# Kernel optimization log

Hardware: AMD Instinct MI355X
Metric: run time of the kernel (lower is better)

## Reference

```python
import jax, jax.numpy as jnp
import numpy as np

NEG_FILL = jnp.finfo(jnp.float32).min  # stands in for tf.float64.min (overflows to -inf in f32)


def setup_inputs() -> dict:
    key = jax.random.key(0)
    k0, k1, k2, k3, k4 = jax.random.split(key, 5)
    B, N, E, D = 4, 4096, 1024, 256
    STD = 0.05  # tf.random_normal_initializer default stddev
    inputs = jax.random.normal(k0, (B, N, E), dtype=jnp.float32)
    Wq = STD * jax.random.normal(k1, (E, D), dtype=jnp.float32)
    Wk = STD * jax.random.normal(k2, (E, D), dtype=jnp.float32)
    Wvdown = STD * jax.random.normal(k3, (E, D), dtype=jnp.float32)
    Wvup = STD * jax.random.normal(k4, (D, E), dtype=jnp.float32)
    return {"inputs": inputs, "Wq": Wq, "Wk": Wk, "Wvdown": Wvdown, "Wvup": Wvup}


def reference(inputs, Wq, Wk, Wvdown, Wvup):
    B, N, E = inputs.shape
    D = Wq.shape[1]
    Q = inputs @ Wq                                   # [B, N, D]
    K = inputs @ Wk                                   # [B, N, D]
    score = jnp.einsum("bqd,bkd->bqk", Q, K)          # [B, N, N]
    score = score / jnp.sqrt(jnp.float32(D))
    # tf.linalg.band_part(score, -1, 0): keep lower triangle (causal)
    causal = jnp.tril(jnp.ones((N, N), dtype=bool))
    score = jnp.where(causal, score, 0.0)
    # original quirk: any exactly-zero entry (including masked ones) -> huge negative
    score = jnp.where(score != 0, score, NEG_FILL)
    attn = jax.nn.softmax(score, axis=-1)             # [B, N, N]
    V = inputs @ (Wvdown @ Wvup)                      # low-rank value proj, [B, N, E]
    return attn @ V                                   # [B, N, E]
```

## Files before the change

### kernel.cpp

```cpp
#include <hip/hip_runtime.h>
#include <hip/hip_bf16.h>


typedef __hip_bfloat16 bf16;
typedef __bf16 bf16x4 __attribute__((ext_vector_type(4)));
typedef __bf16 bf16x8 __attribute__((ext_vector_type(8)));
typedef float f32x4 __attribute__((ext_vector_type(4)));

#define BK 32

__device__ __forceinline__ void gload_lds16(const bf16* g, bf16* l) {
    __builtin_amdgcn_global_load_lds(
        (const __attribute__((address_space(1))) unsigned int*)g,
        (__attribute__((address_space(3))) unsigned int*)l, 16, 0, 0);
}

__device__ __forceinline__ void zero_acc(f32x4 acc[4][4]) {
#pragma unroll
    for (int mi = 0; mi < 4; ++mi)
#pragma unroll
        for (int ni = 0; ni < 4; ++ni) {
            f32x4 zf = {0.f, 0.f, 0.f, 0.f};
            acc[mi][ni] = zf;
        }
}

__device__ __forceinline__ void mm_tile(const bf16* __restrict__ Ablk,
                                        const bf16* __restrict__ Bblk,
                                        int lda, int ldb, int kiters,
                                        bf16* As, bf16* Bs, f32x4 acc[4][4]) {
    const int tid  = threadIdx.x;
    const int wave = tid >> 6;
    const int lane = tid & 63;

    const int F0 = wave * 2048 + lane * 16;
    const int F1 = F0 + 1024;
    const int r0 = F0 >> 6, c0 = (F0 & 63) >> 1;
    const int r1 = F1 >> 6, c1 = (F1 & 63) >> 1;
    const bf16* ga0 = Ablk + (size_t)r0 * lda + c0;
    const bf16* ga1 = Ablk + (size_t)r1 * lda + c1;
    const bf16* gb0 = Bblk + (size_t)r0 * ldb + c0;
    const bf16* gb1 = Bblk + (size_t)r1 * ldb + c1;
    bf16* lA0 = (bf16*)((char*)As + F0);
    bf16* lA1 = (bf16*)((char*)As + F1);
    bf16* lB0 = (bf16*)((char*)Bs + F0);
    bf16* lB1 = (bf16*)((char*)Bs + F1);

    const int waveM = wave >> 1, waveN = wave & 1;
    const int mrow = waveM * 64 + (lane & 15);
    const int nrow = waveN * 64 + (lane & 15);
    const int koff = (lane >> 4) * 8;

    for (int it = 0; it < kiters; ++it) {
        gload_lds16(ga0, lA0);
        gload_lds16(ga1, lA1);
        gload_lds16(gb0, lB0);
        gload_lds16(gb1, lB1);
        ga0 += BK; ga1 += BK; gb0 += BK; gb1 += BK;
        __syncthreads();

        bf16x8 af[4], bfr[4];
#pragma unroll
        for (int mi = 0; mi < 4; ++mi)
            af[mi] = *(const bf16x8*)(As + (mrow + mi * 16) * BK + koff);
#pragma unroll
        for (int ni = 0; ni < 4; ++ni)
            bfr[ni] = *(const bf16x8*)(Bs + (nrow + ni * 16) * BK + koff);
#pragma unroll
        for (int mi = 0; mi < 4; ++mi)
#pragma unroll
            for (int ni = 0; ni < 4; ++ni)
                acc[mi][ni] = __builtin_amdgcn_mfma_f32_16x16x32_bf16(
                    af[mi], bfr[ni], acc[mi][ni], 0, 0, 0);
        __syncthreads();
    }
}

__global__ __launch_bounds__(256, 2) void k_gemm_plain(
    const bf16* __restrict__ A, long long aBatch,
    const bf16* __restrict__ BT, long long bBatch,
    bf16* __restrict__ C, long long cBatch,
    int lda, int ldb, int ldc, int kiters) {
    __shared__ __align__(16) bf16 As[128 * BK];
    __shared__ __align__(16) bf16 Bs[128 * BK];
    const int nBase = blockIdx.x * 128;
    const int mBase = blockIdx.y * 128;
    const int z = blockIdx.z;
    const bf16* Ab = A + (size_t)z * aBatch + (size_t)mBase * lda;
    const bf16* Bb = BT + (size_t)z * bBatch + (size_t)nBase * ldb;

    f32x4 acc[4][4];
    zero_acc(acc);
    mm_tile(Ab, Bb, lda, ldb, kiters, As, Bs, acc);

    const int tid = threadIdx.x, wave = tid >> 6, lane = tid & 63;
    const int waveM = wave >> 1, waveN = wave & 1;
    const int quad = lane >> 4, cno = lane & 15;
    bf16* Cb = C + (size_t)z * cBatch;
#pragma unroll
    for (int mi = 0; mi < 4; ++mi) {
        int row0 = mBase + waveM * 64 + mi * 16 + quad * 4;
#pragma unroll
        for (int ni = 0; ni < 4; ++ni) {
            int col = nBase + waveN * 64 + ni * 16 + cno;
#pragma unroll
            for (int r = 0; r < 4; ++r)
                Cb[(size_t)(row0 + r) * ldc + col] = __float2bfloat16(acc[mi][ni][r]);
        }
    }
}

#define P_BATCH 8650752ll
__global__ __launch_bounds__(256, 2) void k_score(
    const bf16* __restrict__ Qm, const bf16* __restrict__ Km,
    bf16* __restrict__ P, float* __restrict__ lsum) {
    const int f = blockIdx.x, b = blockIdx.z;
    int qt = (int)((sqrtf(8.f * (float)f + 1.f) - 1.f) * 0.5f);
    while ((qt + 1) * (qt + 2) / 2 <= f) ++qt;
    while (qt * (qt + 1) / 2 > f) --qt;
    const int kt = f - qt * (qt + 1) / 2;

    __shared__ __align__(16) bf16 As[128 * BK];
    __shared__ __align__(16) bf16 Bs[128 * BK];

    const bf16* Ab = Qm + ((size_t)b * 4096 + (size_t)qt * 128) * 256;
    const bf16* Bb = Km + ((size_t)b * 4096 + (size_t)kt * 128) * 256;

    f32x4 acc[4][4];
    zero_acc(acc);
    mm_tile(Ab, Bb, 256, 256, 256 / BK, As, Bs, acc);

    const int tid = threadIdx.x, wave = tid >> 6, lane = tid & 63;
    const int waveM = wave >> 1, waveN = wave & 1;
    const int quad = lane >> 4, cno = lane & 15;
    const int pitch = (qt + 1) * 128;
    bf16* Pb = P + b * P_BATCH + (size_t)16384 * (qt * (qt + 1) / 2);
    float* lb = lsum + b * 4096;
#pragma unroll
    for (int mi = 0; mi < 4; ++mi) {
        const int lq0 = waveM * 64 + mi * 16 + quad * 4;
        float rs[4] = {0.f, 0.f, 0.f, 0.f};
#pragma unroll
        for (int ni = 0; ni < 4; ++ni) {
            const int cn = waveN * 64 + ni * 16 + cno;
            const int gk = kt * 128 + cn;
#pragma unroll
            for (int r = 0; r < 4; ++r) {
                const int gq = qt * 128 + lq0 + r;
                float s = acc[mi][ni][r] * 0.0625f;
                float p = (gk <= gq && s != 0.0f) ? __expf(s) : 0.0f;
                bf16 pb = __float2bfloat16(p);
                Pb[(size_t)(lq0 + r) * pitch + gk] = pb;
                rs[r] += __bfloat162float(pb);
            }
        }
#pragma unroll
        for (int r = 0; r < 4; ++r) {
            float v = rs[r];
            v += __shfl_xor(v, 1);
            v += __shfl_xor(v, 2);
            v += __shfl_xor(v, 4);
            v += __shfl_xor(v, 8);
            if (cno == 0) atomicAdd(&lb[qt * 128 + lq0 + r], v);
        }
    }
}

__global__ __launch_bounds__(256, 2) void k_pv(
    const bf16* __restrict__ P, const bf16* __restrict__ VT,
    const float* __restrict__ lsum, float* __restrict__ Out) {
    __shared__ __align__(16) bf16 As[128 * BK];
    __shared__ __align__(16) bf16 Bs[128 * BK];
    const int dvBase = blockIdx.x * 128;
    const int pair = blockIdx.y;
    const int b = blockIdx.z;
    const int tid = threadIdx.x, wave = tid >> 6, lane = tid & 63;
    const int waveM = wave >> 1, waveN = wave & 1;
    const int quad = lane >> 4, cno = lane & 15;

    const bf16* Bb = VT + ((size_t)b * 1024 + dvBase) * 4096;
    float* Ob = Out + (size_t)b * 4096 * 1024;
    const float* lb = lsum + b * 4096;

    for (int half = 0; half < 2; ++half) {
        const int qt = half ? pair : (31 - pair);
        const int pitch = (qt + 1) * 128;
        const bf16* Ab = P + b * P_BATCH + (size_t)16384 * (qt * (qt + 1) / 2);

        f32x4 acc[4][4];
        zero_acc(acc);
        mm_tile(Ab, Bb, pitch, 4096, (qt + 1) * (128 / BK), As, Bs, acc);

#pragma unroll
        for (int mi = 0; mi < 4; ++mi) {
            const int lq0 = waveM * 64 + mi * 16 + quad * 4;
#pragma unroll
            for (int r = 0; r < 4; ++r) {
                const int gq = qt * 128 + lq0 + r;
                const float inv = 1.0f / lb[gq];
#pragma unroll
                for (int ni = 0; ni < 4; ++ni) {
                    const int col = dvBase + waveN * 64 + ni * 16 + cno;
                    Ob[(size_t)gq * 1024 + col] = acc[mi][ni][r] * inv;
                }
            }
        }
    }
}

__global__ void k_cast(const float4* __restrict__ in, bf16* __restrict__ out,
                       int n4) {
    int i = blockIdx.x * 256 + threadIdx.x;
    if (i >= n4) return;
    float4 v = in[i];
    bf16x4 o;
    o[0] = (__bf16)v.x; o[1] = (__bf16)v.y; o[2] = (__bf16)v.z; o[3] = (__bf16)v.w;
    *(bf16x4*)(out + 4 * (size_t)i) = o;
}

__global__ void k_transpose(const float* __restrict__ in, bf16* __restrict__ out,
                            int n, int mask, int shift, int tstride) {
    int idx = blockIdx.x * 256 + threadIdx.x;
    if (idx >= n) return;
    out[idx] = __float2bfloat16(in[(size_t)(idx & mask) * tstride + (idx >> shift)]);
}

extern "C" void kernel_launch(void* const* d_in, const int* in_sizes, int n_in,
                              void* d_out, int out_size, void* d_ws, size_t ws_size,
                              hipStream_t stream) {
    const int B = 4, N = 4096, E = 1024, D = 256;
    const float* X   = (const float*)d_in[0];
    const float* Wq  = (const float*)d_in[1];
    const float* Wk  = (const float*)d_in[2];
    const float* Wvd = (const float*)d_in[3];
    const float* Wvu = (const float*)d_in[4];
    float* out = (float*)d_out;

    const long long MiB = 1ll << 20;
    char* ws = (char*)d_ws;
    bf16* Xb     = (bf16*)(ws);
    bf16* WqT    = (bf16*)(ws + 32 * MiB);
    bf16* WkT    = (bf16*)(ws + 32 * MiB + 524288);
    bf16* WvdT   = (bf16*)(ws + 32 * MiB + 1048576);
    bf16* WvupT  = (bf16*)(ws + 32 * MiB + 1572864);
    bf16* P      = (bf16*)(ws);
    bf16* Qm     = (bf16*)(ws + 66 * MiB);
    bf16* Km     = (bf16*)(ws + 74 * MiB);
    bf16* Vd     = (bf16*)(ws + 82 * MiB);
    bf16* VT     = (bf16*)(ws + 90 * MiB);
    float* lsum  = (float*)(ws + 122 * MiB);

    const int n4 = B * N * E / 4;
    k_cast<<<(n4 + 255) / 256, 256, 0, stream>>>((const float4*)X, Xb, n4);
    k_transpose<<<1024, 256, 0, stream>>>(Wq,  WqT,  E * D, 1023, 10, 256);
    k_transpose<<<1024, 256, 0, stream>>>(Wk,  WkT,  E * D, 1023, 10, 256);
    k_transpose<<<1024, 256, 0, stream>>>(Wvd, WvdT, E * D, 1023, 10, 256);
    k_transpose<<<1024, 256, 0, stream>>>(Wvu, WvupT, D * E, 255, 8, 1024);
    hipMemsetAsync(lsum, 0, (size_t)B * N * sizeof(float), stream);

    k_gemm_plain<<<dim3(D / 128, (B * N) / 128, 3), 256, 0, stream>>>(
        Xb, 0, WqT, (long long)D * E, Qm, (long long)B * N * D,
        E, E, D, E / BK);

    k_gemm_plain<<<dim3(N / 128, E / 128, B), 256, 0, stream>>>(
        WvupT, 0, Vd, (long long)N * D, VT, (long long)E * N,
        D, D, N, D / BK);

    k_score<<<dim3(528, 1, B), 256, 0, stream>>>(Qm, Km, P, lsum);

    k_pv<<<dim3(E / 128, 16, B), 256, 0, stream>>>(P, VT, lsum, out);
}
```

Baseline: 347.7 us.

## Double-buffer LDS in GEMM tiles and remap PV blocks to one q-tile each

The shared GEMM tile loop now uses two LDS buffers. The next K-slice's global-to-LDS loads are issued before computing on the current one, with explicit vmcnt waits and barriers, so memory latency overlaps MFMA work. The PV kernel is changed from one block handling a pair of q-tiles (long and short) to 1024 independent blocks, each handling one q-tile. A rotation mapping spreads heavy and light tiles across the launch order. LDS use doubles, to 32KB per block, which may reduce occupancy, and balancing in PV now relies on the hardware scheduler instead of the explicit pairing.

```diff
diff --git a/kernel.cpp b/kernel.cpp
--- a/kernel.cpp
+++ b/kernel.cpp
@@ -8,6 +8,7 @@
 typedef float f32x4 __attribute__((ext_vector_type(4)));
 
 #define BK 32
+#define HALF_BYTES 8192
 
 __device__ __forceinline__ void gload_lds16(const bf16* g, bf16* l) {
     __builtin_amdgcn_global_load_lds(
@@ -23,6 +24,26 @@
             f32x4 zf = {0.f, 0.f, 0.f, 0.f};
             acc[mi][ni] = zf;
         }
+}
+
+__device__ __forceinline__ void compute_step(const bf16* As, const bf16* Bs,
+                                             int cur, int mrow, int nrow,
+                                             int koff, f32x4 acc[4][4]) {
+    const bf16* Ar = (const bf16*)((const char*)As + cur * HALF_BYTES);
+    const bf16* Br = (const bf16*)((const char*)Bs + cur * HALF_BYTES);
+    bf16x8 af[4], bfr[4];
+#pragma unroll
+    for (int mi = 0; mi < 4; ++mi)
+        af[mi] = *(const bf16x8*)(Ar + (mrow + mi * 16) * BK + koff);
+#pragma unroll
+    for (int ni = 0; ni < 4; ++ni)
+        bfr[ni] = *(const bf16x8*)(Br + (nrow + ni * 16) * BK + koff);
+#pragma unroll
+    for (int mi = 0; mi < 4; ++mi)
+#pragma unroll
+        for (int ni = 0; ni < 4; ++ni)
+            acc[mi][ni] = __builtin_amdgcn_mfma_f32_16x16x32_bf16(
+                af[mi], bfr[ni], acc[mi][ni], 0, 0, 0);
 }
 
 __device__ __forceinline__ void mm_tile(const bf16* __restrict__ Ablk,
@@ -41,39 +62,51 @@
     const bf16* ga1 = Ablk + (size_t)r1 * lda + c1;
     const bf16* gb0 = Bblk + (size_t)r0 * ldb + c0;
     const bf16* gb1 = Bblk + (size_t)r1 * ldb + c1;
-    bf16* lA0 = (bf16*)((char*)As + F0);
-    bf16* lA1 = (bf16*)((char*)As + F1);
-    bf16* lB0 = (bf16*)((char*)Bs + F0);
-    bf16* lB1 = (bf16*)((char*)Bs + F1);
 
     const int waveM = wave >> 1, waveN = wave & 1;
     const int mrow = waveM * 64 + (lane & 15);
     const int nrow = waveN * 64 + (lane & 15);
     const int koff = (lane >> 4) * 8;
 
-    for (int it = 0; it < kiters; ++it) {
-        gload_lds16(ga0, lA0);
-        gload_lds16(ga1, lA1);
-        gload_lds16(gb0, lB0);
-        gload_lds16(gb1, lB1);
+    gload_lds16(ga0, (bf16*)((char*)As + F0));
+    gload_lds16(ga1, (bf16*)((char*)As + F1));
+    gload_lds16(gb0, (bf16*)((char*)Bs + F0));
+    gload_lds16(gb1, (bf16*)((char*)Bs + F1));
+    ga0 += BK; ga1 += BK; gb0 += BK; gb1 += BK;
+
+    int cur = 0;
+    for (int it = 0; it < kiters - 1; ++it) {
+        const int nxt = cur ^ 1;
+        char* Ad = (char*)As + nxt * HALF_BYTES;
+        char* Bd = (char*)Bs + nxt * HALF_BYTES;
+        gload_lds16(ga0, (bf16*)(Ad + F0));
+        gload_lds16(ga1, (bf16*)(Ad + F1));
+        gload_lds16(gb0, (bf16*)(Bd + F0));
+        gload_lds16(gb1, (bf16*)(Bd + F1));
         ga0 += BK; ga1 += BK; gb0 += BK; gb1 += BK;
-        __syncthreads();
-
-        bf16x8 af[4], bfr[4];
-#pragma unroll
-        for (int mi = 0; mi < 4; ++mi)
-            af[mi] = *(const bf16x8*)(As + (mrow + mi * 16) * BK + koff);
-#pragma unroll
-        for (int ni = 0; ni < 4; ++ni)
-            bfr[ni] = *(const bf16x8*)(Bs + (nrow + ni * 16) * BK + koff);
-#pragma unroll
-        for (int mi = 0; mi < 4; ++mi)
-#pragma unroll
-            for (int ni = 0; ni < 4; ++ni)
-                acc[mi][ni] = __builtin_amdgcn_mfma_f32_16x16x32_bf16(
-                    af[mi], bfr[ni], acc[mi][ni], 0, 0, 0);
-        __syncthreads();
+
+        __builtin_amdgcn_sched_barrier(0);
+        asm volatile("s_waitcnt vmcnt(4)" ::: "memory");
+        __builtin_amdgcn_sched_barrier(0);
+        __builtin_amdgcn_s_barrier();
+        __builtin_amdgcn_sched_barrier(0);
+
+        compute_step(As, Bs, cur, mrow, nrow, koff, acc);
+
+        __builtin_amdgcn_sched_barrier(0);
+        asm volatile("s_waitcnt lgkmcnt(0)" ::: "memory");
+        __builtin_amdgcn_sched_barrier(0);
+        __builtin_amdgcn_s_barrier();
+        __builtin_amdgcn_sched_barrier(0);
+        cur = nxt;
     }
+
+    __builtin_amdgcn_sched_barrier(0);
+    asm volatile("s_waitcnt vmcnt(0)" ::: "memory");
+    __builtin_amdgcn_sched_barrier(0);
+    __builtin_amdgcn_s_barrier();
+    __builtin_amdgcn_sched_barrier(0);
+    compute_step(As, Bs, cur, mrow, nrow, koff, acc);
 }
 
 __global__ __launch_bounds__(256, 2) void k_gemm_plain(
@@ -81,8 +114,8 @@
     const bf16* __restrict__ BT, long long bBatch,
     bf16* __restrict__ C, long long cBatch,
     int lda, int ldb, int ldc, int kiters) {
-    __shared__ __align__(16) bf16 As[128 * BK];
-    __shared__ __align__(16) bf16 Bs[128 * BK];
+    __shared__ __align__(16) bf16 As[2 * 128 * BK];
+    __shared__ __align__(16) bf16 Bs[2 * 128 * BK];
     const int nBase = blockIdx.x * 128;
     const int mBase = blockIdx.y * 128;
     const int z = blockIdx.z;
@@ -120,8 +153,8 @@
     while (qt * (qt + 1) / 2 > f) --qt;
     const int kt = f - qt * (qt + 1) / 2;
 
-    __shared__ __align__(16) bf16 As[128 * BK];
-    __shared__ __align__(16) bf16 Bs[128 * BK];
+    __shared__ __align__(16) bf16 As[2 * 128 * BK];
+    __shared__ __align__(16) bf16 Bs[2 * 128 * BK];
 
     const bf16* Ab = Qm + ((size_t)b * 4096 + (size_t)qt * 128) * 256;
     const bf16* Bb = Km + ((size_t)b * 4096 + (size_t)kt * 128) * 256;
@@ -169,11 +202,19 @@
 __global__ __launch_bounds__(256, 2) void k_pv(
     const bf16* __restrict__ P, const bf16* __restrict__ VT,
     const float* __restrict__ lsum, float* __restrict__ Out) {
-    __shared__ __align__(16) bf16 As[128 * BK];
-    __shared__ __align__(16) bf16 Bs[128 * BK];
-    const int dvBase = blockIdx.x * 128;
-    const int pair = blockIdx.y;
-    const int b = blockIdx.z;
+    __shared__ __align__(16) bf16 As[2 * 128 * BK];
+    __shared__ __align__(16) bf16 Bs[2 * 128 * BK];
+    const int l = blockIdx.x;
+    const int dv = l >> 7;
+    const int w = l & 127;
+    const int b = w >> 5;
+    const int u = w & 31;
+    const int x = u & 7;
+    const int k = u >> 3;
+    const int m = (k + (dv >> 1)) & 3;
+    const int qt = (m == 0) ? x : (m == 1) ? (15 - x)
+                 : (m == 2) ? (16 + x) : (31 - x);
+    const int dvBase = dv * 128;
     const int tid = threadIdx.x, wave = tid >> 6, lane = tid & 63;
     const int waveM = wave >> 1, waveN = wave & 1;
     const int quad = lane >> 4, cno = lane & 15;
@@ -182,27 +223,24 @@
     float* Ob = Out + (size_t)b * 4096 * 1024;
     const float* lb = lsum + b * 4096;
 
-    for (int half = 0; half < 2; ++half) {
-        const int qt = half ? pair : (31 - pair);
-        const int pitch = (qt + 1) * 128;
-        const bf16* Ab = P + b * P_BATCH + (size_t)16384 * (qt * (qt + 1) / 2);
-
-        f32x4 acc[4][4];
-        zero_acc(acc);
-        mm_tile(Ab, Bb, pitch, 4096, (qt + 1) * (128 / BK), As, Bs, acc);
-
-#pragma unroll
-        for (int mi = 0; mi < 4; ++mi) {
-            const int lq0 = waveM * 64 + mi * 16 + quad * 4;
-#pragma unroll
-            for (int r = 0; r < 4; ++r) {
-                const int gq = qt * 128 + lq0 + r;
-                const float inv = 1.0f / lb[gq];
-#pragma unroll
-                for (int ni = 0; ni < 4; ++ni) {
-                    const int col = dvBase + waveN * 64 + ni * 16 + cno;
-                    Ob[(size_t)gq * 1024 + col] = acc[mi][ni][r] * inv;
-                }
+    const int pitch = (qt + 1) * 128;
+    const bf16* Ab = P + b * P_BATCH + (size_t)16384 * (qt * (qt + 1) / 2);
+
+    f32x4 acc[4][4];
+    zero_acc(acc);
+    mm_tile(Ab, Bb, pitch, 4096, (qt + 1) * (128 / BK), As, Bs, acc);
+
+#pragma unroll
+    for (int mi = 0; mi < 4; ++mi) {
+        const int lq0 = waveM * 64 + mi * 16 + quad * 4;
+#pragma unroll
+        for (int r = 0; r < 4; ++r) {
+            const int gq = qt * 128 + lq0 + r;
+            const float inv = 1.0f / lb[gq];
+#pragma unroll
+            for (int ni = 0; ni < 4; ++ni) {
+                const int col = dvBase + waveN * 64 + ni * 16 + cno;
+                Ob[(size_t)gq * 1024 + col] = acc[mi][ni][r] * inv;
             }
         }
     }
@@ -268,5 +306,5 @@
 
     k_score<<<dim3(528, 1, B), 256, 0, stream>>>(Qm, Km, P, lsum);
 
-    k_pv<<<dim3(E / 128, 16, B), 256, 0, stream>>>(P, VT, lsum, out);
-}
+    k_pv<<<dim3(1024, 1, 1), 256, 0, stream>>>(P, VT, lsum, out);
+}
```

New measurement: 331.6 us. 1.05x faster.
